# Kernel optimization log

Hardware: AMD Instinct MI355X
Metric: run time of the kernel (lower is better)

## Reference

```python
import jax, jax.numpy as jnp
import numpy as np

B, T, IN, H, OUT = 64, 32, 256, 512, 256
M, W, R = 256, 64, 4            # nr_cells, cell_size, read_heads
NN_IN = IN + R * W              # 512
NN_OUT = H + R * W              # 768
IFACE = R * W + 3 * W + 5 * R + 3  # 471
CLIP = 20.0
DELTA = 1e-6


def setup_inputs():
    key = jax.random.key(0)
    ks = jax.random.split(key, 10)
    s = 0.05
    bound = float(np.sqrt(6.0 / (B * H + 2 * H)))  # xavier_uniform on (2,B,H)
    return {
        'x': jax.random.normal(ks[0], (B, T, IN), jnp.float32),
        'h0': jax.random.uniform(ks[1], (2, B, H), jnp.float32, -bound, bound),
        'Wih0': jax.random.normal(ks[2], (4 * H, NN_IN), jnp.float32) * s,
        'Whh0': jax.random.normal(ks[3], (4 * H, H), jnp.float32) * s,
        'bih0': jnp.zeros((4 * H,), jnp.float32),
        'bhh0': jnp.zeros((4 * H,), jnp.float32),
        'Wih1': jax.random.normal(ks[4], (4 * H, H), jnp.float32) * s,
        'Whh1': jax.random.normal(ks[5], (4 * H, H), jnp.float32) * s,
        'bih1': jnp.zeros((4 * H,), jnp.float32),
        'bhh1': jnp.zeros((4 * H,), jnp.float32),
        'Wif': jax.random.normal(ks[6], (IFACE, H), jnp.float32) * s,
        'bif': jnp.zeros((IFACE,), jnp.float32),
        'Wout': jax.random.normal(ks[7], (OUT, NN_OUT), jnp.float32) * s,
        'bout': jnp.zeros((OUT,), jnp.float32),
    }


def _lstm_cell(x, h, c, Wih, Whh, bih, bhh):
    g = x @ Wih.T + bih + h @ Whh.T + bhh
    i, f, gg, o = jnp.split(g, 4, axis=1)  # torch gate order i,f,g,o
    c = jax.nn.sigmoid(f) * c + jax.nn.sigmoid(i) * jnp.tanh(gg)
    h = jax.nn.sigmoid(o) * jnp.tanh(c)
    return h, c


def _content_weights(mem, keys, strengths):
    # mem: (b,M,W), keys: (b,K,W), strengths: (b,K) -> softmax over M
    mem_n = mem / (jnp.linalg.norm(mem, axis=2, keepdims=True) + DELTA)
    key_n = keys / (jnp.linalg.norm(keys, axis=2, keepdims=True) + DELTA)
    sim = jnp.einsum('bkw,bmw->bkm', key_n, mem_n)
    return jax.nn.softmax(sim * strengths[..., None], axis=2)


def _memory_step(xi, mem, link, prec, rw, ww, usage):
    b = xi.shape[0]
    o = 0
    rk = jnp.tanh(xi[:, :R * W].reshape(b, R, W)); o = R * W
    rs = jax.nn.softplus(xi[:, o:o + R]); o += R
    wk = jnp.tanh(xi[:, o:o + W]).reshape(b, 1, W); o += W
    ws = jax.nn.softplus(xi[:, o])[:, None]; o += 1
    ev = jax.nn.sigmoid(xi[:, o:o + W]); o += W
    wv = jnp.tanh(xi[:, o:o + W]); o += W
    fg = jax.nn.sigmoid(xi[:, o:o + R]); o += R
    ag = jax.nn.sigmoid(xi[:, o])[:, None]; o += 1
    wg = jax.nn.sigmoid(xi[:, o])[:, None]; o += 1
    rm = jax.nn.softmax(xi[:, o:o + 3 * R].reshape(b, R, 3), axis=2)

    # usage update (uses OLD read/write weights); single write head
    usage = usage + (1.0 - usage) * ww
    psi = jnp.prod(1.0 - fg[:, :, None] * rw, axis=1)
    usage = usage * psi

    # write content addressing on OLD memory
    wcw = _content_weights(mem, wk, ws)[:, 0]  # (b,M)

    # allocation by ascending sort of usage (exclusive cumprod)
    u = DELTA + (1.0 - DELTA) * usage
    phi = jnp.argsort(u, axis=1)
    sorted_u = jnp.take_along_axis(u, phi, axis=1)
    excl = jnp.cumprod(jnp.concatenate([jnp.ones((b, 1), u.dtype), sorted_u], axis=1), axis=1)[:, :-1]
    sorted_alloc = (1.0 - sorted_u) * excl
    alloc = jnp.take_along_axis(sorted_alloc, jnp.argsort(phi, axis=1), axis=1)

    ww = wg * (ag * alloc + (1.0 - ag) * wcw)  # (b,M)

    # erase + write
    mem = mem * (1.0 - ww[:, :, None] * ev[:, None, :]) + ww[:, :, None] * wv[:, None, :]

    # temporal link matrix + precedence
    prev_scale = 1.0 - ww[:, :, None] - ww[:, None, :]
    link = prev_scale * link + ww[:, :, None] * prec[:, None, :]
    link = link * (1.0 - jnp.eye(M, dtype=link.dtype))
    prec = (1.0 - ww.sum(axis=1, keepdims=True)) * prec + ww

    # read: directional weights use NEW link and OLD read weights; content uses NEW memory
    rcw = _content_weights(mem, rk, rs)               # (b,R,M)
    fwd = jnp.einsum('bij,brj->bri', link, rw)
    bwd = jnp.einsum('brj,bji->bri', rw, link)
    rw = rm[:, :, 0:1] * bwd + rm[:, :, 1:2] * fwd + rm[:, :, 2:3] * rcw
    rvec = jnp.einsum('brm,bmw->brw', rw, mem).reshape(b, R * W)
    return rvec, mem, link, prec, rw, ww, usage


def reference(x, h0, Wih0, Whh0, bih0, bhh0, Wih1, Whh1, bih1, bhh1, Wif, bif, Wout, bout):
    b = x.shape[0]
    lr0 = jnp.zeros((b, R * W), x.dtype)  # initial last_read; NOTE: source concatenates this
    # initial zero last_read to EVERY timestep's controller input (inputs built upfront)
    carry0 = (h0[0], h0[0], h0[1], h0[1],
              jnp.full((b, M, W), DELTA, x.dtype),   # memory
              jnp.zeros((b, M, M), x.dtype),          # link matrix
              jnp.zeros((b, M), x.dtype),             # precedence
              jnp.full((b, R, M), DELTA, x.dtype),    # read weights
              jnp.full((b, M), DELTA, x.dtype),       # write weights
              jnp.zeros((b, M), x.dtype))             # usage

    def step(carry, x_t):
        h0_, c0_, h1_, c1_, mem, link, prec, rw, ww, usage = carry
        inp = jnp.concatenate([x_t, lr0], axis=1)
        h0_, c0_ = _lstm_cell(inp, h0_, c0_, Wih0, Whh0, bih0, bhh0)
        h1_, c1_ = _lstm_cell(h0_, h1_, c1_, Wih1, Whh1, bih1, bhh1)
        out = jnp.clip(h1_, -CLIP, CLIP)
        xi = out @ Wif.T + bif
        rvec, mem, link, prec, rw, ww, usage = _memory_step(xi, mem, link, prec, rw, ww, usage)
        o_t = jnp.concatenate([out, rvec], axis=1)  # (b, NN_OUT)
        return (h0_, c0_, h1_, c1_, mem, link, prec, rw, ww, usage), o_t

    _, ys = jax.lax.scan(step, carry0, jnp.swapaxes(x, 0, 1))  # (T,b,NN_OUT)
    outputs = jnp.tanh(ys) @ Wout.T + bout  # Dropout(p=0) -> Tanh -> Linear
    return jnp.swapaxes(outputs, 0, 1)      # (b,T,OUT)
```

## Files before the change

### kernel.cpp

```cpp
#include <hip/hip_runtime.h>
#include <hip/hip_bf16.h>
#include <math.h>


typedef __bf16 bf16_t;
typedef __attribute__((ext_vector_type(8))) __bf16 bf16x8;
typedef __attribute__((ext_vector_type(4))) float f32x4;

#define B_    64
#define T_    32
#define IN_   256
#define H_    512
#define M_    256
#define W_    64
#define R_    4
#define IFACE_ 471
#define DELTA_ 1e-6f

#define OFF_H0SEQ  (0L)
#define SZ_H0SEQ   (32L*64*512*2)
#define OFF_OUTSEQ (OFF_H0SEQ + SZ_H0SEQ)
#define SZ_OUTSEQ  (32L*64*512*2)
#define OFF_H0BUF  (OFF_OUTSEQ + SZ_OUTSEQ)
#define SZ_HBUF    (2L*64*512*2)
#define OFF_H1BUF  (OFF_H0BUF + SZ_HBUF)
#define OFF_XI     (OFF_H1BUF + SZ_HBUF)
#define SZ_XI      (32L*64*480*4)
#define OFF_RVEC   (OFF_XI + SZ_XI)
#define SZ_RVEC    (32L*64*256*4)
#define OFF_YBF    (OFF_RVEC + SZ_RVEC)
#define SZ_YBF     (32L*64*768*2)
#define OFF_BAR    (OFF_YBF + SZ_YBF)
#define SZ_BAR     (256L)
#define OFF_XB     (OFF_BAR + SZ_BAR)
#define SZ_XB      (64L*32*256*2)
#define OFF_H0B    (OFF_XB + SZ_XB)
#define SZ_H0B     (2L*64*512*2)
#define OFF_W0     (OFF_H0B + SZ_H0B)
#define SZ_W       (2048L*512*2)
#define OFF_W1     (OFF_W0 + SZ_W)
#define OFF_W2     (OFF_W1 + SZ_W)
#define OFF_W3     (OFF_W2 + SZ_W)
#define OFF_WIF    (OFF_W3 + SZ_W)
#define SZ_WIF     (480L*512*2)
#define OFF_WOUTB  (OFF_WIF + SZ_WIF)
#define SZ_WOUTB   (256L*768*2)
#define OFF_BS0    (OFF_WOUTB + SZ_WOUTB)
#define SZ_BS      (2048L*4)
#define OFF_BS1    (OFF_BS0 + SZ_BS)
#define OFF_BIF    (OFF_BS1 + SZ_BS)
#define SZ_BIF     (2048L)
#define OFF_BOUTF  (OFF_BIF + SZ_BIF)
#define SZ_BOUTF   (1024L)
#define OFF_FLG    (OFF_BOUTF + SZ_BOUTF)
#define SZ_FLG     (4096L)

__device__ __forceinline__ float frcp(float x){ return __builtin_amdgcn_rcpf(x); }
__device__ __forceinline__ float fsqrt_(float x){ return __builtin_amdgcn_sqrtf(x); }
__device__ __forceinline__ float sigf(float x){ return frcp(1.0f + __expf(-x)); }
__device__ __forceinline__ float tanh_f(float x){
  float xc = fminf(fmaxf(x, -44.0f), 44.0f);
  float t = __expf(2.0f * xc);
  return (t - 1.0f) * frcp(t + 1.0f);
}
__device__ __forceinline__ float softplusf(float x){
  return fmaxf(x, 0.0f) + __logf(1.0f + __expf(-fabsf(x)));
}
__device__ __forceinline__ float wred(float v){
  #pragma unroll
  for (int off = 32; off; off >>= 1) v += __shfl_xor(v, off, 64);
  return v;
}
__device__ __forceinline__ float ldin(const void* p, long i, int mf){
  return mf ? ((const float*)p)[i] : (float)((const bf16_t*)p)[i];
}

__device__ __forceinline__ unsigned flag_ld(const unsigned* p){
  return __hip_atomic_load(p, __ATOMIC_RELAXED, __HIP_MEMORY_SCOPE_AGENT);
}

__device__ __forceinline__ void flagbar(unsigned* flg, int bid, unsigned tgt,
                                        int tid, int lane, int wv){
  __syncthreads();
  if (tid == 0)
    __hip_atomic_store(flg + (size_t)bid*16, tgt, __ATOMIC_RELEASE,
                       __HIP_MEMORY_SCOPE_AGENT);
  if (wv == 0){
    for (;;){
      unsigned f = flag_ld(flg + (size_t)lane*16);
      if (__all(f >= tgt)) break;
      __builtin_amdgcn_s_sleep(2);
    }
    __builtin_amdgcn_fence(__ATOMIC_ACQUIRE, "agent");
  }
  __syncthreads();
}

__global__ void k_detect(const unsigned short* __restrict__ x16,
                         int* __restrict__ flag, unsigned* __restrict__ bar,
                         unsigned* __restrict__ flg){
  __shared__ int cnt;
  if (threadIdx.x == 0){ cnt = 0; bar[0] = 0u; bar[1] = 0u; }
  for (int i = threadIdx.x; i < 1024; i += 256) flg[i] = 0u;
  __syncthreads();
  unsigned short u = x16[threadIdx.x * 2];
  int e = (u >> 7) & 0xFF;
  if (e >= 0x88) atomicAdd(&cnt, 1);
  __syncthreads();
  if (threadIdx.x == 0) *flag = (cnt > 16) ? 1 : 0;
}

__global__ void k_convert(const void* x, const void* h0, const void* Wih0,
                          const void* Whh0, const void* bih0, const void* bhh0,
                          const void* Wih1, const void* Whh1, const void* bih1,
                          const void* bhh1, const void* Wif, const void* bif,
                          const void* Wout, const void* bout,
                          bf16_t* __restrict__ xb, bf16_t* __restrict__ h0b,
                          bf16_t* __restrict__ h0buf, bf16_t* __restrict__ h1buf,
                          bf16_t* __restrict__ W0, bf16_t* __restrict__ W1,
                          bf16_t* __restrict__ W2, bf16_t* __restrict__ W3,
                          bf16_t* __restrict__ Wifp, bf16_t* __restrict__ Woutb,
                          float* __restrict__ bs0, float* __restrict__ bs1,
                          float* __restrict__ bifp, float* __restrict__ boutf,
                          const int* __restrict__ flag)
{
  const int mf = *flag;
  const long stride = (long)gridDim.x * blockDim.x;
  long i0 = (long)blockIdx.x * blockDim.x + threadIdx.x;
  switch (blockIdx.y){
  case 0: for (long i = i0; i < 64L*32*256; i += stride) xb[i] = (bf16_t)ldin(x, i, mf); break;
  case 1: for (long i = i0; i < 2L*64*512; i += stride){
            float v = ldin(h0, i, mf); bf16_t bb = (bf16_t)v; h0b[i] = bb;
            if (i < 64*512) h0buf[i] = bb; else h1buf[i - 64*512] = bb;
          } break;
  case 2: for (long i = i0; i < 2048L*512; i += stride) W0[i] = (bf16_t)ldin(Wih0, i, mf); break;
  case 3: for (long i = i0; i < 2048L*512; i += stride) W1[i] = (bf16_t)ldin(Whh0, i, mf); break;
  case 4: for (long i = i0; i < 2048L*512; i += stride) W2[i] = (bf16_t)ldin(Wih1, i, mf); break;
  case 5: for (long i = i0; i < 2048L*512; i += stride) W3[i] = (bf16_t)ldin(Whh1, i, mf); break;
  case 6: for (long i = i0; i < 480L*512; i += stride){
            long r = i >> 9;
            Wifp[i] = (r < IFACE_) ? (bf16_t)ldin(Wif, i, mf) : (bf16_t)0.0f;
          } break;
  case 7: for (long i = i0; i < 256L*768; i += stride) Woutb[i] = (bf16_t)ldin(Wout, i, mf); break;
  case 8:
    for (long i = i0; i < 2048; i += stride){
      bs0[i] = ldin(bih0, i, mf) + ldin(bhh0, i, mf);
      bs1[i] = ldin(bih1, i, mf) + ldin(bhh1, i, mf);
    }
    for (long i = i0; i < 480; i += stride) bifp[i] = (i < IFACE_) ? ldin(bif, i, mf) : 0.0f;
    for (long i = i0; i < 256; i += stride) boutf[i] = ldin(bout, i, mf);
    break;
  }
}

__device__ __forceinline__ void softmax256_wave(float* a, int lane){
  float v0=a[lane], v1=a[64+lane], v2=a[128+lane], v3=a[192+lane];
  float mx = fmaxf(fmaxf(v0,v1), fmaxf(v2,v3));
  #pragma unroll
  for (int off=32; off; off>>=1) mx = fmaxf(mx, __shfl_xor(mx, off, 64));
  v0=__expf(v0-mx); v1=__expf(v1-mx); v2=__expf(v2-mx); v3=__expf(v3-mx);
  float s = v0+v1+v2+v3;
  #pragma unroll
  for (int off=32; off; off>>=1) s += __shfl_xor(s, off, 64);
  float inv = frcp(s);
  a[lane]=v0*inv; a[64+lane]=v1*inv; a[128+lane]=v2*inv; a[192+lane]=v3*inv;
}

struct ProdShm {
  bf16_t wpool[66560];
  float  cst[64][16];
  float  bias[4][16];
};
struct ConsShm {
  float smem[256][65];
  float rkn4r[4][65][4];
  float wkn[64], ev_[64], wvv[64];
  float rs_[4], fg_[4], rm_[4][3];
  float wsS, agS, wgS, wwsumS;
  float invn[256], wcw[256];
  float usage[256], uu[256], su[256], scanA[256];
  int   rank_[256];
  int   rankP[2][256];
  float ww_[256], prec_[256];
  float rw_[4][256];
  float rw4[256][4];
  float fwd_[4][256], bwd_[4][256], rcw_[4][256];
  bf16_t rwb[4][264];
  float p4cT[4][264];
  float p5cT[5][4][264];
  float rvp[16][4][64];
};
union ShUnion { ProdShm p; ConsShm c; };

__global__ __launch_bounds__(1024) void k_main(
    const bf16_t* __restrict__ xb, const bf16_t* __restrict__ h0b,
    const bf16_t* __restrict__ W0, const bf16_t* __restrict__ W1,
    const bf16_t* __restrict__ W2, const bf16_t* __restrict__ W3,
    const float* __restrict__ bs0, const float* __restrict__ bs1,
    const bf16_t* __restrict__ Wifp, const float* __restrict__ bifp,
    bf16_t* __restrict__ h0buf, bf16_t* __restrict__ h1buf,
    bf16_t* __restrict__ h0seq, bf16_t* __restrict__ outseq,
    float* __restrict__ XI, float* __restrict__ RVEC,
    unsigned* __restrict__ flg)
{
  __shared__ ShUnion sh;
  const int bid = blockIdx.x;
  const int tid = threadIdx.x, lane = tid & 63, wv = tid >> 6;
  const int m16 = lane & 15, q = lane >> 4;

  if (bid < 64){
    ProdShm& P = sh.p;
    const int layer = bid >> 5;
    const int u0 = (bid & 31) * 16;

    if (!layer){
      for (int i = tid; i < 64*32; i += 1024){
        int rl = i >> 5, c8 = (i & 31)*8;
        int grow = (rl >> 4)*512 + u0 + (rl & 15);
        *(bf16x8*)&P.wpool[rl*264 + c8] = *(const bf16x8*)(W0 + (size_t)grow*512 + c8);
      }
      for (int i = tid; i < 64*64; i += 1024){
        int rl = i >> 6, c8 = (i & 63)*8;
        int grow = (rl >> 4)*512 + u0 + (rl & 15);
        *(bf16x8*)&P.wpool[16896 + rl*520 + c8] = *(const bf16x8*)(W1 + (size_t)grow*512 + c8);
      }
    } else {
      for (int i = tid; i < 64*64; i += 1024){
        int rl = i >> 6, c8 = (i & 63)*8;
        int grow = (rl >> 4)*512 + u0 + (rl & 15);
        *(bf16x8*)&P.wpool[rl*520 + c8]         = *(const bf16x8*)(W2 + (size_t)grow*512 + c8);
        *(bf16x8*)&P.wpool[33280 + rl*520 + c8] = *(const bf16x8*)(W3 + (size_t)grow*512 + c8);
      }
    }
    for (int i = tid; i < 64*16; i += 1024){
      int b = i >> 4, n = i & 15;
      P.cst[b][n] = (float)h0b[layer*(64*512) + b*512 + u0 + n];
    }
    if (tid < 64){
      int G = tid >> 4, n = tid & 15;
      const float* bs = layer ? bs1 : bs0;
      P.bias[G][n] = bs[G*512 + u0 + n];
    }
    __syncthreads();

    bf16_t* hbuf = layer ? h1buf : h0buf;

    for (int ps = 0; ps <= 33; ++ps){
      if (wv < 4){
        const int t = layer ? (ps - 1) : ps;
        const bool active = layer ? (ps >= 1 && ps <= 32) : (ps < 32);
        if (active){
          const int p = t & 1;
          const bf16_t* hin = hbuf + p*(64*512);
          bf16_t* hout = hbuf + (p^1)*(64*512);
          const int b0 = wv * 16;

          f32x4 acc[4];
          #pragma unroll
          for (int G = 0; G < 4; ++G){ float bv = P.bias[G][m16]; acc[G] = (f32x4){bv,bv,bv,bv}; }

          if (!layer){
            #pragma unroll 2
            for (int kt = 0; kt < 8; ++kt){
              bf16x8 a = *(const bf16x8*)(xb + ((size_t)(b0+m16)*T_ + t)*IN_ + kt*32 + q*8);
              #pragma unroll
              for (int G = 0; G < 4; ++G)
                acc[G] = __builtin_amdgcn_mfma_f32_16x16x32_bf16(
                    a, *(const bf16x8*)&P.wpool[(G*16+m16)*264 + kt*32 + q*8], acc[G], 0, 0, 0);
            }
            #pragma unroll 4
            for (int kt = 0; kt < 16; ++kt){
              bf16x8 a = *(const bf16x8*)(hin + (b0+m16)*512 + kt*32 + q*8);
              #pragma unroll
              for (int G = 0; G < 4; ++G)
                acc[G] = __builtin_amdgcn_mfma_f32_16x16x32_bf16(
                    a, *(const bf16x8*)&P.wpool[16896 + (G*16+m16)*520 + kt*32 + q*8], acc[G], 0, 0, 0);
            }
          } else {
            #pragma unroll 4
            for (int kt = 0; kt < 16; ++kt){
              bf16x8 a = *(const bf16x8*)(h0seq + ((size_t)t*64 + b0+m16)*512 + kt*32 + q*8);
              #pragma unroll
              for (int G = 0; G < 4; ++G)
                acc[G] = __builtin_amdgcn_mfma_f32_16x16x32_bf16(
                    a, *(const bf16x8*)&P.wpool[(G*16+m16)*520 + kt*32 + q*8], acc[G], 0, 0, 0);
            }
            #pragma unroll 4
            for (int kt = 0; kt < 16; ++kt){
              bf16x8 a = *(const bf16x8*)(hin + (b0+m16)*512 + kt*32 + q*8);
              #pragma unroll
              for (int G = 0; G < 4; ++G)
                acc[G] = __builtin_amdgcn_mfma_f32_16x16x32_bf16(
                    a, *(const bf16x8*)&P.wpool[33280 + (G*16+m16)*520 + kt*32 + q*8], acc[G], 0, 0, 0);
            }
          }
          #pragma unroll
          for (int v = 0; v < 4; ++v){
            int b = b0 + q*4 + v;
            float gi = acc[0][v], gf = acc[1][v], gg = acc[2][v], go = acc[3][v];
            float c_ = sigf(gf)*P.cst[b][m16] + sigf(gi)*tanh_f(gg);
            P.cst[b][m16] = c_;
            float h = sigf(go)*tanh_f(c_);
            bf16_t hb = (bf16_t)h;
            hout[b*512 + u0 + m16] = hb;
            if (!layer) h0seq[((size_t)t*64 + b)*512 + u0 + m16] = hb;
            else        outseq[((size_t)t*64 + b)*512 + u0 + m16] = hb;
          }
        }
      } else if (wv < 8 && ps >= 2 && bid < 30){
        const int t2 = ps - 2;
        const int b0 = (wv - 4) * 16;
        const int r = bid*16 + m16;
        float bv = bifp[r];
        f32x4 acc = {bv,bv,bv,bv};
        const bf16_t* arow = outseq + ((size_t)t2*64 + b0 + m16)*512 + q*8;
        const bf16_t* brow = Wifp + (size_t)r*512 + q*8;
        #pragma unroll 4
        for (int kt = 0; kt < 16; ++kt){
          acc = __builtin_amdgcn_mfma_f32_16x16x32_bf16(
              *(const bf16x8*)(arow + kt*32), *(const bf16x8*)(brow + kt*32), acc, 0, 0, 0);
        }
        #pragma unroll
        for (int v = 0; v < 4; ++v)
          XI[((size_t)t2*64 + b0 + q*4 + v)*480 + r] = acc[v];
      }
      flagbar(flg, bid, (unsigned)(ps + 1), tid, lane, wv);
    }
  } else {
    ConsShm& S = sh.c;
    const int b = bid - 64;
    const int quad = lane >> 4, li = lane & 15;

    const int orow = wv*16 + li;
    bf16x8 rowL[8], colL[8];
    #pragma unroll
    for (int ch = 0; ch < 8; ++ch)
      #pragma unroll
      for (int z = 0; z < 8; ++z){ rowL[ch][z] = (bf16_t)0.0f; colL[ch][z] = (bf16_t)0.0f; }

    const int mQ = tid >> 2, q4 = tid & 3;
    float mr[16];
    #pragma unroll
    for (int z = 0; z < 16; ++z) mr[z] = DELTA_;

    int off0 = -1, off1 = -1, off2 = -1;
    if (wv < 4)            off0 = wv*64 + lane;
    else if (wv == 4)      off0 = 260 + lane;
    else if (wv == 5)      off0 = 325 + lane;
    else if (wv == 6)      off0 = 389 + lane;
    else if (wv == 7){
      if (lane < 4)        off0 = 256 + lane;
      else if (lane == 4)  off0 = 324;
      else if (lane < 9)   off0 = 453 + (lane - 5);
      else if (lane == 9)  off0 = 457;
      else if (lane == 10) off0 = 458;
      else if (lane >= 16 && lane < 20){
        off0 = 459 + (lane - 16)*3; off1 = off0 + 1; off2 = off0 + 2;
      }
    }

    if (tid < 256){
      S.ww_[tid] = DELTA_; S.usage[tid] = 0.0f; S.prec_[tid] = 0.0f;
      S.invn[tid] = 1.0f/(fsqrt_(64.0f*DELTA_*DELTA_) + DELTA_);
      #pragma unroll
      for (int r = 0; r < 4; ++r) S.rw_[r][tid] = DELTA_;
    }
    for (int i = tid; i < 4*264; i += 1024) ((bf16_t*)S.rwb)[i] = (bf16_t)DELTA_;
    for (int i = tid; i < 256*65; i += 1024) ((float*)S.smem)[i] = DELTA_;
    __syncthreads();

    if (wv == 0){
      for (;;){
        unsigned f = flag_ld(flg + (size_t)lane*16);
        if (__all(f >= 3u)) break;
        __builtin_amdgcn_s_sleep(2);
      }
      __builtin_amdgcn_fence(__ATOMIC_ACQUIRE, "agent");
    }
    __syncthreads();
    float x0 = 0.0f, x1 = 0.0f, x2 = 0.0f;
    {
      const float* xp = XI + (size_t)b*480;
      if (off0 >= 0) x0 = xp[off0];
      if (off1 >= 0){ x1 = xp[off1]; x2 = xp[off2]; }
    }

    for (int t = 0; t < 32; ++t){
      if (wv < 4){
        float v = tanh_f(x0);
        float s = wred(v*v);
        float vn = v * frcp(fsqrt_(s) + DELTA_);
        #pragma unroll
        for (int g = 0; g < 4; ++g) S.rkn4r[g][lane][wv] = vn;
      } else if (wv == 4){
        float v = tanh_f(x0);
        float s = wred(v*v);
        S.wkn[lane] = v * frcp(fsqrt_(s) + DELTA_);
      } else if (wv == 5){ S.ev_[lane] = sigf(x0);
      } else if (wv == 6){ S.wvv[lane] = tanh_f(x0);
      } else if (wv == 7){
        if (lane < 4)        S.rs_[lane] = softplusf(x0);
        else if (lane == 4)  S.wsS = softplusf(x0);
        else if (lane < 9)   S.fg_[lane-5] = sigf(x0);
        else if (lane == 9)  S.agS = sigf(x0);
        else if (lane == 10) S.wgS = sigf(x0);
        else if (lane >= 16 && lane < 20){
          int r = lane - 16;
          float mx = fmaxf(x0, fmaxf(x1, x2));
          float e0 = __expf(x0-mx), e1 = __expf(x1-mx), e2 = __expf(x2-mx);
          float inv = frcp(e0+e1+e2);
          S.rm_[r][0]=e0*inv; S.rm_[r][1]=e1*inv; S.rm_[r][2]=e2*inv;
        }
      }
      __syncthreads();

      if (tid < 256){
        int m = tid;
        float us = S.usage[m] + (1.0f - S.usage[m])*S.ww_[m];
        float psi = (1.0f - S.fg_[0]*S.rw_[0][m]) * (1.0f - S.fg_[1]*S.rw_[1][m])
                  * (1.0f - S.fg_[2]*S.rw_[2][m]) * (1.0f - S.fg_[3]*S.rw_[3][m]);
        us *= psi;
        S.usage[m] = us;
        S.uu[m] = DELTA_ + (1.0f - DELTA_)*us;
      }
      { float acc = 0.0f;
        #pragma unroll
        for (int it = 0; it < 16; ++it){
          int w = q4*16 + it;
          acc += mr[it] * S.wkn[w];
        }
        S.p4cT[q4][mQ] = acc; }
      __syncthreads();

      if (wv == 0){
        #pragma unroll
        for (int z = 0; z < 4; ++z){
          int m = z*64 + lane;
          S.wcw[m] = S.wsS * (S.p4cT[0][m] + S.p4cT[1][m] + S.p4cT[2][m] + S.p4cT[3][m]) * S.invn[m];
        }
        softmax256_wave(S.wcw, lane);
      } else if (tid >= 512){
        const int idx = tid - 512;
        const int i = idx & 255, half = idx >> 8;
        const float ui = S.uu[i];
        int cnt = 0;
        #pragma unroll 8
        for (int k = 0; k < 32; ++k){
          f32x4 u4 = *(const f32x4*)&S.uu[half*128 + k*4];
          #pragma unroll
          for (int z = 0; z < 4; ++z){
            int j = half*128 + k*4 + z; float uj = u4[z];
            cnt += (uj < ui || (uj == ui && j < i)) ? 1 : 0;
          }
        }
        S.rankP[half][i] = cnt;
      }
      __syncthreads();

      if (tid < 256){
        int rank = S.rankP[0][tid] + S.rankP[1][tid];
        S.rank_[tid] = rank;
        S.su[rank] = S.uu[tid];
      }
      __syncthreads();

      if (wv == 0){
        int base = lane*4;
        float v0 = S.su[base], v1 = S.su[base+1], v2 = S.su[base+2];
        float p1 = v0*v1, p2 = p1*v2, p3 = p2*S.su[base+3];
        float sc = p3;
        #pragma unroll
        for (int off = 1; off < 64; off <<= 1){
          float n = __shfl_up(sc, off, 64);
          if (lane >= off) sc *= n;
        }
        float exch = __shfl_up(sc, 1, 64);
        if (lane == 0) exch = 1.0f;
        S.scanA[base] = exch; S.scanA[base+1] = exch*v0;
        S.scanA[base+2] = exch*p1; S.scanA[base+3] = exch*p2;
      }
      __syncthreads();

      { float al = (1.0f - S.uu[mQ]) * S.scanA[S.rank_[mQ]];
        float wm = S.wgS*(S.agS*al + (1.0f - S.agS)*S.wcw[mQ]);
        if (q4 == 0) S.ww_[mQ] = wm;
        float s2 = 0.0f, sr0 = 0.0f, sr1 = 0.0f, sr2 = 0.0f, sr3 = 0.0f;
        #pragma unroll
        for (int it = 0; it < 16; ++it){
          int w = q4*16 + it;
          float mn = mr[it]*(1.0f - wm*S.ev_[w]) + wm*S.wvv[w];
          mr[it] = mn;
          S.smem[mQ][w] = mn;
          s2 += mn*mn;
          f32x4 rk = *(const f32x4*)&S.rkn4r[q4][w][0];
          sr0 += mn*rk[0]; sr1 += mn*rk[1]; sr2 += mn*rk[2]; sr3 += mn*rk[3];
        }
        S.p5cT[0][q4][mQ] = s2;
        S.p5cT[1][q4][mQ] = sr0; S.p5cT[2][q4][mQ] = sr1;
        S.p5cT[3][q4][mQ] = sr2; S.p5cT[4][q4][mQ] = sr3; }
      __syncthreads();

      if (tid < 256){
        int m = tid;
        float s2 = S.p5cT[0][0][m] + S.p5cT[0][1][m] + S.p5cT[0][2][m] + S.p5cT[0][3][m];
        float inv = frcp(fsqrt_(s2) + DELTA_);
        S.invn[m] = inv;
        #pragma unroll
        for (int r = 0; r < 4; ++r){
          float sr = S.p5cT[r+1][0][m] + S.p5cT[r+1][1][m] + S.p5cT[r+1][2][m] + S.p5cT[r+1][3][m];
          S.rcw_[r][m] = S.rs_[r]*sr*inv;
        }
      } else if (wv == 4){
        float s = wred(S.ww_[lane] + S.ww_[64+lane] + S.ww_[128+lane] + S.ww_[192+lane]);
        if (lane == 0) S.wwsumS = s;
      }
      { const float wown = S.ww_[orow], pown = S.prec_[orow];
        const float alpha = 1.0f - wown;
        f32x4 facc = {0,0,0,0}, bacc = {0,0,0,0};
        #pragma unroll
        for (int ch = 0; ch < 8; ++ch){
          const int cbase = ch*32 + quad*8;
          bf16x8 rwf = *(const bf16x8*)&S.rwb[li & 3][cbase];
          f32x4 wA = *(const f32x4*)&S.ww_[cbase];
          f32x4 wB = *(const f32x4*)&S.ww_[cbase+4];
          f32x4 pA = *(const f32x4*)&S.prec_[cbase];
          f32x4 pB = *(const f32x4*)&S.prec_[cbase+4];
          float wcf[8] = {wA[0],wA[1],wA[2],wA[3],wB[0],wB[1],wB[2],wB[3]};
          float pcf[8] = {pA[0],pA[1],pA[2],pA[3],pB[0],pB[1],pB[2],pB[3]};
          bf16x8 rl = rowL[ch];
          bf16x8 cl = colL[ch];
          #pragma unroll
          for (int jj = 0; jj < 8; ++jj){
            const int c = cbase + jj;
            float s = alpha - wcf[jj];
            float vr = s*(float)rl[jj] + wown*pcf[jj];
            float vc = s*(float)cl[jj] + wcf[jj]*pown;
            if (c == orow){ vr = 0.0f; vc = 0.0f; }
            rl[jj] = (bf16_t)vr;
            cl[jj] = (bf16_t)vc;
          }
          rowL[ch] = rl; colL[ch] = cl;
          facc = __builtin_amdgcn_mfma_f32_16x16x32_bf16(rl, rwf, facc, 0, 0, 0);
          bacc = __builtin_amdgcn_mfma_f32_16x16x32_bf16(rwf, cl, bacc, 0, 0, 0);
        }
        if (li < 4){
          #pragma unroll
          for (int z = 0; z < 4; ++z) S.fwd_[li][wv*16 + quad*4 + z] = facc[z];
        }
        if (quad == 0){
          #pragma unroll
          for (int z = 0; z < 4; ++z) S.bwd_[z][wv*16 + li] = bacc[z];
        }
      }
      __syncthreads();

      if (wv < 4) softmax256_wave(S.rcw_[wv], lane);
      else if (tid >= 512 && tid < 768){
        int m = tid - 512;
        float p = (1.0f - S.wwsumS)*S.prec_[m] + S.ww_[m];
        S.prec_[m] = p;
      } else if (wv == 15 && t < 31){
        const unsigned tgt = (unsigned)(t + 4);
        for (;;){
          unsigned f = flag_ld(flg + (size_t)lane*16);
          if (__all(f >= tgt)) break;
          __builtin_amdgcn_s_sleep(2);
        }
        __builtin_amdgcn_fence(__ATOMIC_ACQUIRE, "agent");
      }
      __syncthreads();

      if (t < 31 && off0 >= 0){
        const float* xp = XI + ((size_t)(t+1)*64 + b)*480;
        x0 = xp[off0];
        if (off1 >= 0){ x1 = xp[off1]; x2 = xp[off2]; }
      }
      { const int r = tid >> 8, m = tid & 255;
        float v = S.rm_[r][0]*S.bwd_[r][m] + S.rm_[r][1]*S.fwd_[r][m] + S.rm_[r][2]*S.rcw_[r][m];
        S.rw_[r][m] = v;
        S.rw4[m][r] = v;
        S.rwb[r][m] = (bf16_t)v;
      }
      __syncthreads();

      { float r0 = 0, r1 = 0, r2 = 0, r3 = 0;
        #pragma unroll
        for (int k = 0; k < 16; ++k){
          int m = wv*16 + k;
          f32x4 r4 = *(const f32x4*)&S.rw4[m][0];
          float mv = S.smem[m][lane];
          r0 += r4[0]*mv; r1 += r4[1]*mv; r2 += r4[2]*mv; r3 += r4[3]*mv;
        }
        S.rvp[wv][0][lane] = r0; S.rvp[wv][1][lane] = r1;
        S.rvp[wv][2][lane] = r2; S.rvp[wv][3][lane] = r3; }
      __syncthreads();

      if (tid < 256){
        const int w = tid & 63, r = tid >> 6;
        float v = 0.0f;
        #pragma unroll
        for (int c = 0; c < 16; ++c) v += S.rvp[c][r][w];
        RVEC[((size_t)t*64 + b)*256 + tid] = v;
      }
    }
  }
}

__global__ void k_tanhy(const bf16_t* __restrict__ outseq, const float* __restrict__ RVEC,
                        bf16_t* __restrict__ Y){
  const int n = 2048*768;
  for (int i = blockIdx.x*blockDim.x + threadIdx.x; i < n; i += gridDim.x*blockDim.x){
    int row = i / 768, j = i - row*768;
    float v = (j < 512) ? (float)outseq[(size_t)row*512 + j] : RVEC[(size_t)row*256 + (j - 512)];
    Y[i] = (bf16_t)tanh_f(v);
  }
}

__global__ __launch_bounds__(256,1) void k_out(
    const bf16_t* __restrict__ Y, const bf16_t* __restrict__ Woutb,
    const float* __restrict__ boutf, void* __restrict__ dout,
    const int* __restrict__ flag)
{
  const int mf = *flag;
  const int mt = blockIdx.x;
  const int tid = threadIdx.x, lane = tid & 63, wv = tid >> 6;
  const int nt = blockIdx.y*4 + wv;
  const int m16 = lane & 15, q = lane >> 4;
  const int o = nt*16 + m16;
  float bv = boutf[o];
  f32x4 acc = {bv,bv,bv,bv};
  const bf16_t* arow = Y + (size_t)(mt*16 + m16)*768 + q*8;
  const bf16_t* brow = Woutb + (size_t)o*768 + q*8;
  for (int kt = 0; kt < 24; ++kt){
    acc = __builtin_amdgcn_mfma_f32_16x16x32_bf16(
        *(const bf16x8*)(arow + kt*32), *(const bf16x8*)(brow + kt*32), acc, 0, 0, 0);
  }
  #pragma unroll
  for (int v = 0; v < 4; ++v){
    int row = mt*16 + q*4 + v;
    int b = row & 63, t = row >> 6;
    size_t idx = ((size_t)b*T_ + t)*256 + o;
    if (mf) ((float*)dout)[idx] = acc[v];
    else    ((bf16_t*)dout)[idx] = (bf16_t)acc[v];
  }
}

extern "C" void kernel_launch(void* const* d_in, const int* in_sizes, int n_in,
                              void* d_out, int out_size, void* d_ws, size_t ws_size,
                              hipStream_t stream)
{
  char* ws = (char*)d_ws;
  bf16_t* H0SEQ  = (bf16_t*)(ws + OFF_H0SEQ);
  bf16_t* OUTSEQ = (bf16_t*)(ws + OFF_OUTSEQ);
  bf16_t* H0BUF  = (bf16_t*)(ws + OFF_H0BUF);
  bf16_t* H1BUF  = (bf16_t*)(ws + OFF_H1BUF);
  float*  XI     = (float*) (ws + OFF_XI);
  float*  RVEC   = (float*) (ws + OFF_RVEC);
  bf16_t* YBF    = (bf16_t*)(ws + OFF_YBF);
  unsigned* BAR  = (unsigned*)(ws + OFF_BAR);
  int*    FLAG   = (int*)   (ws + OFF_BAR + 8);
  bf16_t* XB     = (bf16_t*)(ws + OFF_XB);
  bf16_t* H0B    = (bf16_t*)(ws + OFF_H0B);
  bf16_t* W0     = (bf16_t*)(ws + OFF_W0);
  bf16_t* W1     = (bf16_t*)(ws + OFF_W1);
  bf16_t* W2     = (bf16_t*)(ws + OFF_W2);
  bf16_t* W3     = (bf16_t*)(ws + OFF_W3);
  bf16_t* WIFP   = (bf16_t*)(ws + OFF_WIF);
  bf16_t* WOUTB  = (bf16_t*)(ws + OFF_WOUTB);
  float*  BS0    = (float*) (ws + OFF_BS0);
  float*  BS1    = (float*) (ws + OFF_BS1);
  float*  BIFP   = (float*) (ws + OFF_BIF);
  float*  BOUTF  = (float*) (ws + OFF_BOUTF);
  unsigned* FLG  = (unsigned*)(ws + OFF_FLG);

  k_detect<<<1, 256, 0, stream>>>((const unsigned short*)d_in[0], FLAG, BAR, FLG);
  k_convert<<<dim3(256, 9), 256, 0, stream>>>(
      d_in[0], d_in[1], d_in[2], d_in[3], d_in[4], d_in[5], d_in[6],
      d_in[7], d_in[8], d_in[9], d_in[10], d_in[11], d_in[12], d_in[13],
      XB, H0B, H0BUF, H1BUF, W0, W1, W2, W3, WIFP, WOUTB,
      BS0, BS1, BIFP, BOUTF, FLAG);
  k_main<<<128, 1024, 0, stream>>>(XB, H0B, W0, W1, W2, W3, BS0, BS1,
                                   WIFP, BIFP, H0BUF, H1BUF, H0SEQ, OUTSEQ,
                                   XI, RVEC, FLG);
  k_tanhy<<<512, 256, 0, stream>>>(OUTSEQ, RVEC, YBF);
  k_out<<<dim3(128, 4), 256, 0, stream>>>(YBF, WOUTB, BOUTF, d_out, FLAG);
}
```

Before: 1.014 ms.

## Drop per-thread column link copy and memory registers, transpose link via LDS tiles

Removes the colL register copy of the link matrix columns and the mr[] register copy of memory rows. Memory rows are now read from and written to shared memory directly. The backward link product is rebuilt each step by staging row tiles of the link matrix in a shared-memory transpose buffer (unioned with scratch arrays) across 8 sub-iterations. The aim is to cut VGPR pressure and redundant link-update arithmetic. The cost is 16 extra block barriers per timestep plus strided LDS reads on the serial consumer path.

```diff
diff --git a/kernel.cpp b/kernel.cpp
--- a/kernel.cpp
+++ b/kernel.cpp
@@ -173,22 +173,31 @@
 };
 struct ConsShm {
   float smem[256][65];
-  float rkn4r[4][65][4];
   float wkn[64], ev_[64], wvv[64];
   float rs_[4], fg_[4], rm_[4][3];
   float wsS, agS, wgS, wwsumS;
-  float invn[256], wcw[256];
-  float usage[256], uu[256], su[256], scanA[256];
-  int   rank_[256];
-  int   rankP[2][256];
+  float invn[256];
+  float usage[256];
   float ww_[256], prec_[256];
   float rw_[4][256];
   float rw4[256][4];
   float fwd_[4][256], bwd_[4][256], rcw_[4][256];
   bf16_t rwb[4][264];
-  float p4cT[4][264];
-  float p5cT[5][4][264];
-  float rvp[16][4][64];
+  union {
+    struct {
+      float rkn4r[4][65][4];
+      float wcw[256];
+      float uu[256];
+      float su[256];
+      float scanA[256];
+      int   rank_[256];
+      int   rankP[2][256];
+      float p4cT[4][264];
+      float p5cT[5][4][264];
+      float rvp[16][4][64];
+    } a;
+    bf16_t tls[32][258];
+  } u;
 };
 union ShUnion { ProdShm p; ConsShm c; };
 
@@ -332,16 +341,13 @@
     const int quad = lane >> 4, li = lane & 15;
 
     const int orow = wv*16 + li;
-    bf16x8 rowL[8], colL[8];
+    bf16x8 rowL[8];
     #pragma unroll
     for (int ch = 0; ch < 8; ++ch)
       #pragma unroll
-      for (int z = 0; z < 8; ++z){ rowL[ch][z] = (bf16_t)0.0f; colL[ch][z] = (bf16_t)0.0f; }
+      for (int z = 0; z < 8; ++z) rowL[ch][z] = (bf16_t)0.0f;
 
     const int mQ = tid >> 2, q4 = tid & 3;
-    float mr[16];
-    #pragma unroll
-    for (int z = 0; z < 16; ++z) mr[z] = DELTA_;
 
     int off0 = -1, off1 = -1, off2 = -1;
     if (wv < 4)            off0 = wv*64 + lane;
@@ -391,7 +397,7 @@
         float s = wred(v*v);
         float vn = v * frcp(fsqrt_(s) + DELTA_);
         #pragma unroll
-        for (int g = 0; g < 4; ++g) S.rkn4r[g][lane][wv] = vn;
+        for (int g = 0; g < 4; ++g) S.u.a.rkn4r[g][lane][wv] = vn;
       } else if (wv == 4){
         float v = tanh_f(x0);
         float s = wred(v*v);
@@ -421,53 +427,54 @@
                   * (1.0f - S.fg_[2]*S.rw_[2][m]) * (1.0f - S.fg_[3]*S.rw_[3][m]);
         us *= psi;
         S.usage[m] = us;
-        S.uu[m] = DELTA_ + (1.0f - DELTA_)*us;
+        S.u.a.uu[m] = DELTA_ + (1.0f - DELTA_)*us;
       }
       { float acc = 0.0f;
         #pragma unroll
         for (int it = 0; it < 16; ++it){
           int w = q4*16 + it;
-          acc += mr[it] * S.wkn[w];
-        }
-        S.p4cT[q4][mQ] = acc; }
+          acc += S.smem[mQ][w] * S.wkn[w];
+        }
+        S.u.a.p4cT[q4][mQ] = acc; }
       __syncthreads();
 
       if (wv == 0){
         #pragma unroll
         for (int z = 0; z < 4; ++z){
           int m = z*64 + lane;
-          S.wcw[m] = S.wsS * (S.p4cT[0][m] + S.p4cT[1][m] + S.p4cT[2][m] + S.p4cT[3][m]) * S.invn[m];
-        }
-        softmax256_wave(S.wcw, lane);
+          S.u.a.wcw[m] = S.wsS * (S.u.a.p4cT[0][m] + S.u.a.p4cT[1][m]
+                                + S.u.a.p4cT[2][m] + S.u.a.p4cT[3][m]) * S.invn[m];
+        }
+        softmax256_wave(S.u.a.wcw, lane);
       } else if (tid >= 512){
         const int idx = tid - 512;
         const int i = idx & 255, half = idx >> 8;
-        const float ui = S.uu[i];
+        const float ui = S.u.a.uu[i];
         int cnt = 0;
         #pragma unroll 8
         for (int k = 0; k < 32; ++k){
-          f32x4 u4 = *(const f32x4*)&S.uu[half*128 + k*4];
+          f32x4 u4 = *(const f32x4*)&S.u.a.uu[half*128 + k*4];
           #pragma unroll
           for (int z = 0; z < 4; ++z){
             int j = half*128 + k*4 + z; float uj = u4[z];
             cnt += (uj < ui || (uj == ui && j < i)) ? 1 : 0;
           }
         }
-        S.rankP[half][i] = cnt;
+        S.u.a.rankP[half][i] = cnt;
       }
       __syncthreads();
 
       if (tid < 256){
-        int rank = S.rankP[0][tid] + S.rankP[1][tid];
-        S.rank_[tid] = rank;
-        S.su[rank] = S.uu[tid];
+        int rank = S.u.a.rankP[0][tid] + S.u.a.rankP[1][tid];
+        S.u.a.rank_[tid] = rank;
+        S.u.a.su[rank] = S.u.a.uu[tid];
       }
       __syncthreads();
 
       if (wv == 0){
         int base = lane*4;
-        float v0 = S.su[base], v1 = S.su[base+1], v2 = S.su[base+2];
-        float p1 = v0*v1, p2 = p1*v2, p3 = p2*S.su[base+3];
+        float v0 = S.u.a.su[base], v1 = S.u.a.su[base+1], v2 = S.u.a.su[base+2];
+        float p1 = v0*v1, p2 = p1*v2, p3 = p2*S.u.a.su[base+3];
         float sc = p3;
         #pragma unroll
         for (int off = 1; off < 64; off <<= 1){
@@ -476,38 +483,39 @@
         }
         float exch = __shfl_up(sc, 1, 64);
         if (lane == 0) exch = 1.0f;
-        S.scanA[base] = exch; S.scanA[base+1] = exch*v0;
-        S.scanA[base+2] = exch*p1; S.scanA[base+3] = exch*p2;
-      }
-      __syncthreads();
-
-      { float al = (1.0f - S.uu[mQ]) * S.scanA[S.rank_[mQ]];
-        float wm = S.wgS*(S.agS*al + (1.0f - S.agS)*S.wcw[mQ]);
+        S.u.a.scanA[base] = exch; S.u.a.scanA[base+1] = exch*v0;
+        S.u.a.scanA[base+2] = exch*p1; S.u.a.scanA[base+3] = exch*p2;
+      }
+      __syncthreads();
+
+      { float al = (1.0f - S.u.a.uu[mQ]) * S.u.a.scanA[S.u.a.rank_[mQ]];
+        float wm = S.wgS*(S.agS*al + (1.0f - S.agS)*S.u.a.wcw[mQ]);
         if (q4 == 0) S.ww_[mQ] = wm;
         float s2 = 0.0f, sr0 = 0.0f, sr1 = 0.0f, sr2 = 0.0f, sr3 = 0.0f;
         #pragma unroll
         for (int it = 0; it < 16; ++it){
           int w = q4*16 + it;
-          float mn = mr[it]*(1.0f - wm*S.ev_[w]) + wm*S.wvv[w];
-          mr[it] = mn;
+          float mn = S.smem[mQ][w]*(1.0f - wm*S.ev_[w]) + wm*S.wvv[w];
           S.smem[mQ][w] = mn;
           s2 += mn*mn;
-          f32x4 rk = *(const f32x4*)&S.rkn4r[q4][w][0];
+          f32x4 rk = *(const f32x4*)&S.u.a.rkn4r[q4][w][0];
           sr0 += mn*rk[0]; sr1 += mn*rk[1]; sr2 += mn*rk[2]; sr3 += mn*rk[3];
         }
-        S.p5cT[0][q4][mQ] = s2;
-        S.p5cT[1][q4][mQ] = sr0; S.p5cT[2][q4][mQ] = sr1;
-        S.p5cT[3][q4][mQ] = sr2; S.p5cT[4][q4][mQ] = sr3; }
+        S.u.a.p5cT[0][q4][mQ] = s2;
+        S.u.a.p5cT[1][q4][mQ] = sr0; S.u.a.p5cT[2][q4][mQ] = sr1;
+        S.u.a.p5cT[3][q4][mQ] = sr2; S.u.a.p5cT[4][q4][mQ] = sr3; }
       __syncthreads();
 
       if (tid < 256){
         int m = tid;
-        float s2 = S.p5cT[0][0][m] + S.p5cT[0][1][m] + S.p5cT[0][2][m] + S.p5cT[0][3][m];
+        float s2 = S.u.a.p5cT[0][0][m] + S.u.a.p5cT[0][1][m]
+                 + S.u.a.p5cT[0][2][m] + S.u.a.p5cT[0][3][m];
         float inv = frcp(fsqrt_(s2) + DELTA_);
         S.invn[m] = inv;
         #pragma unroll
         for (int r = 0; r < 4; ++r){
-          float sr = S.p5cT[r+1][0][m] + S.p5cT[r+1][1][m] + S.p5cT[r+1][2][m] + S.p5cT[r+1][3][m];
+          float sr = S.u.a.p5cT[r+1][0][m] + S.u.a.p5cT[r+1][1][m]
+                   + S.u.a.p5cT[r+1][2][m] + S.u.a.p5cT[r+1][3][m];
           S.rcw_[r][m] = S.rs_[r]*sr*inv;
         }
       } else if (wv == 4){
@@ -516,7 +524,7 @@
       }
       { const float wown = S.ww_[orow], pown = S.prec_[orow];
         const float alpha = 1.0f - wown;
-        f32x4 facc = {0,0,0,0}, bacc = {0,0,0,0};
+        f32x4 facc = {0,0,0,0};
         #pragma unroll
         for (int ch = 0; ch < 8; ++ch){
           const int cbase = ch*32 + quad*8;
@@ -528,24 +536,41 @@
           float wcf[8] = {wA[0],wA[1],wA[2],wA[3],wB[0],wB[1],wB[2],wB[3]};
           float pcf[8] = {pA[0],pA[1],pA[2],pA[3],pB[0],pB[1],pB[2],pB[3]};
           bf16x8 rl = rowL[ch];
-          bf16x8 cl = colL[ch];
           #pragma unroll
           for (int jj = 0; jj < 8; ++jj){
             const int c = cbase + jj;
             float s = alpha - wcf[jj];
             float vr = s*(float)rl[jj] + wown*pcf[jj];
-            float vc = s*(float)cl[jj] + wcf[jj]*pown;
-            if (c == orow){ vr = 0.0f; vc = 0.0f; }
+            if (c == orow) vr = 0.0f;
             rl[jj] = (bf16_t)vr;
-            cl[jj] = (bf16_t)vc;
           }
-          rowL[ch] = rl; colL[ch] = cl;
+          rowL[ch] = rl;
           facc = __builtin_amdgcn_mfma_f32_16x16x32_bf16(rl, rwf, facc, 0, 0, 0);
-          bacc = __builtin_amdgcn_mfma_f32_16x16x32_bf16(rwf, cl, bacc, 0, 0, 0);
         }
         if (li < 4){
           #pragma unroll
           for (int z = 0; z < 4; ++z) S.fwd_[li][wv*16 + quad*4 + z] = facc[z];
+        }
+      }
+      __syncthreads();
+
+      { f32x4 bacc = {0,0,0,0};
+        #pragma unroll 1
+        for (int sub = 0; sub < 8; ++sub){
+          if ((wv >> 1) == sub){
+            #pragma unroll
+            for (int ch = 0; ch < 8; ++ch)
+              *(bf16x8*)&S.u.tls[(wv & 1)*16 + li][ch*32 + quad*8] = rowL[ch];
+          }
+          __syncthreads();
+          { bf16x8 rwf = *(const bf16x8*)&S.rwb[li & 3][sub*32 + quad*8];
+            const int x = wv*16 + li;
+            bf16x8 cl;
+            #pragma unroll
+            for (int z = 0; z < 8; ++z) cl[z] = S.u.tls[quad*8 + z][x];
+            bacc = __builtin_amdgcn_mfma_f32_16x16x32_bf16(rwf, cl, bacc, 0, 0, 0);
+          }
+          __syncthreads();
         }
         if (quad == 0){
           #pragma unroll
@@ -591,15 +616,15 @@
           float mv = S.smem[m][lane];
           r0 += r4[0]*mv; r1 += r4[1]*mv; r2 += r4[2]*mv; r3 += r4[3]*mv;
         }
-        S.rvp[wv][0][lane] = r0; S.rvp[wv][1][lane] = r1;
-        S.rvp[wv][2][lane] = r2; S.rvp[wv][3][lane] = r3; }
+        S.u.a.rvp[wv][0][lane] = r0; S.u.a.rvp[wv][1][lane] = r1;
+        S.u.a.rvp[wv][2][lane] = r2; S.u.a.rvp[wv][3][lane] = r3; }
       __syncthreads();
 
       if (tid < 256){
         const int w = tid & 63, r = tid >> 6;
         float v = 0.0f;
         #pragma unroll
-        for (int c = 0; c < 16; ++c) v += S.rvp[c][r][w];
+        for (int c = 0; c < 16; ++c) v += S.u.a.rvp[c][r][w];
         RVEC[((size_t)t*64 + b)*256 + tid] = v;
       }
     }
```

Measured after the change: 972.4 us (median of 2 runs). -4.1%, faster.
